# Optimization experiments

Hardware: AMD Instinct MI355X
Metric: run time of the kernel (lower is better)

The kernel has to match this reference:

```python
import jax, jax.numpy as jnp
import numpy as np

NUM_EXECUTORS = 50
NUM_DAG_FEATURES = 3
EMB_DAG = 16
EMB_GLOB = 16
HIDDEN = [64, 64, 32]
B = 60000            # number of jobs (one per env in the batched rollout)
NODES_PER_JOB = 10
NODE_FEAT = 5


def _init_mlp(key, dims):
    ws, bs = [], []
    for i in range(len(dims) - 1):
        key, k = jax.random.split(key)
        scale = 1.0 / np.sqrt(dims[i])
        ws.append(jax.random.uniform(k, (dims[i], dims[i + 1]), jnp.float32, -scale, scale))
        bs.append(jnp.zeros((dims[i + 1],), jnp.float32))
    return ws, bs


def setup_inputs() -> dict:
    rng = np.random.default_rng(0)
    n_nodes = B * NODES_PER_JOB
    # dag_batch.ptr: job i owns nodes [i*NODES_PER_JOB, (i+1)*NODES_PER_JOB)
    ptr = np.arange(B + 1, dtype=np.int64) * NODES_PER_JOB
    job_indices = rng.permutation(B).astype(np.int64)
    # ragged action counts per job (exec_mask is a prefix mask of length num_exec_acts[i])
    num_exec_acts = rng.integers(1, NUM_EXECUTORS + 1, size=B).astype(np.int64)
    n_sel = num_exec_acts[job_indices]
    T = int(n_sel.sum())
    # per-ragged-row executor index: concat([arange(n) for n in n_sel]), vectorized
    starts = np.cumsum(n_sel) - n_sel
    exec_act_idx = (np.arange(T, dtype=np.int64) - np.repeat(starts, n_sel)).astype(np.int64)

    key = jax.random.key(0)
    k_x, k_hd, k_hg, k_mlp = jax.random.split(key, 4)
    x = jax.random.normal(k_x, (n_nodes, NODE_FEAT), jnp.float32)
    h_dag = jax.random.normal(k_hd, (B, EMB_DAG), jnp.float32)
    h_glob = jax.random.normal(k_hg, (B, EMB_GLOB), jnp.float32)

    in_dim = NUM_DAG_FEATURES + EMB_DAG + EMB_GLOB + 1  # 36
    ws, bs = _init_mlp(k_mlp, [in_dim] + HIDDEN + [1])

    return {
        "x": x,
        "h_dag": h_dag,
        "h_glob": h_glob,
        "ptr": jnp.asarray(ptr),
        "job_indices": jnp.asarray(job_indices),
        "num_exec_acts": jnp.asarray(num_exec_acts),
        "exec_act_idx": jnp.asarray(exec_act_idx),
        "W1": ws[0], "b1": bs[0],
        "W2": ws[1], "b2": bs[1],
        "W3": ws[2], "b3": bs[2],
        "W4": ws[3], "b4": bs[3],
    }


def reference(x, h_dag, h_glob, ptr, job_indices, num_exec_acts, exec_act_idx,
              W1, b1, W2, b2, W3, b3, W4, b4):
    T = exec_act_idx.shape[0]                       # total ragged action rows (static)
    J = job_indices.shape[0]
    # masked gather: dag features at each dag's start node, then select jobs
    x_dag = x[ptr[:-1], :NUM_DAG_FEATURES][job_indices]        # [J, 3]
    h_dag_sel = h_dag[job_indices]                              # [J, 16]
    x_h_dag = jnp.concatenate([x_dag, h_dag_sel], axis=1)       # [J, 19]
    # variable repeat_interleave -> gather by repeated row index
    n_sel = num_exec_acts[job_indices]
    rpt = jnp.repeat(jnp.arange(J), n_sel, total_repeat_length=T)
    x_h_rpt = x_h_dag[rpt]                                      # [T, 19]
    h_glob_rpt = h_glob[rpt]                                    # [T, 16]
    # exec action feature: k / num_executors for the k-th valid executor
    exec_actions = (exec_act_idx.astype(x.dtype) / NUM_EXECUTORS)[:, None]  # [T, 1]
    h = jnp.concatenate([x_h_rpt, h_glob_rpt, exec_actions], axis=1)        # [T, 36]
    h = jax.nn.relu(h @ W1 + b1)
    h = jax.nn.relu(h @ W2 + b2)
    h = jax.nn.relu(h @ W3 + b3)
    scores = (h @ W4 + b4).squeeze(-1)                          # [T]
    return scores
```

## Files before the change

### kernel.cpp

```cpp
#include <hip/hip_runtime.h>

#define TPB 256

using half8  = __attribute__((ext_vector_type(8))) _Float16;
using fp16x2 = __attribute__((ext_vector_type(2))) __fp16;
using f32x4  = __attribute__((ext_vector_type(4))) float;

static __device__ __forceinline__ unsigned short h2u(_Float16 h) {
    union { _Float16 h; unsigned short u; } v; v.h = h; return v.u;
}
static __device__ __forceinline__ unsigned pkrtz(float a, float b) {
    fp16x2 h = __builtin_amdgcn_cvt_pkrtz(a, b);
    return __builtin_bit_cast(unsigned, h);
}
template <int CTRL>
static __device__ __forceinline__ float dppmov(float x) {
    return __int_as_float(__builtin_amdgcn_mov_dpp(__float_as_int(x), CTRL, 0xF, 0xF, true));
}
#define DPP_SWAP 0xB1

__global__ __launch_bounds__(TPB) void k_prep(const float* __restrict__ x,
                                              const float* __restrict__ h_dag,
                                              const float* __restrict__ h_glob,
                                              const int* __restrict__ ptr,
                                              const int* __restrict__ job_indices,
                                              const int* __restrict__ num_exec_acts,
                                              int J, int nb,
                                              unsigned int* __restrict__ feat,
                                              int* __restrict__ bsum, int* __restrict__ jsv,
                                              const float* __restrict__ W1,
                                              const float* __restrict__ b1,
                                              const float* __restrict__ W2,
                                              const float* __restrict__ b2,
                                              const float* __restrict__ W3,
                                              const float* __restrict__ b3,
                                              const float* __restrict__ W4,
                                              uint4* __restrict__ wfrag,
                                              float4* __restrict__ bfrag)
{
    if (blockIdx.x == (unsigned)nb) {
        if (threadIdx.x < 64) {
            int lane = threadIdx.x;
            int n = lane & 15, q = lane >> 4;
#pragma unroll
            for (int nt = 0; nt < 4; nt++) {
#pragma unroll
                for (int s = 0; s < 2; s++) {
                    half8 w1f, w2f;
#pragma unroll
                    for (int jj = 0; jj < 8; jj++) {
                        int ks = s * 32 + q * 8 + jj;
                        w1f[jj] = (ks < 36) ? (_Float16)W1[ks * 64 + nt * 16 + n] : (_Float16)0.0f;
                        w2f[jj] = (_Float16)W2[ks * 64 + nt * 16 + n];
                    }
                    wfrag[(nt * 2 + s) * 64 + lane]     = __builtin_bit_cast(uint4, w1f);
                    wfrag[(8 + nt * 2 + s) * 64 + lane] = __builtin_bit_cast(uint4, w2f);
                }
            }
#pragma unroll
            for (int nt = 0; nt < 2; nt++) {
#pragma unroll
                for (int s = 0; s < 2; s++) {
                    half8 w3f;
#pragma unroll
                    for (int jj = 0; jj < 8; jj++) {
                        int ks = s * 32 + q * 8 + jj;
                        w3f[jj] = (_Float16)W3[ks * 32 + nt * 16 + n];
                    }
                    wfrag[(16 + nt * 2 + s) * 64 + lane] = __builtin_bit_cast(uint4, w3f);
                }
            }
            bfrag[0 * 64 + lane] = make_float4(b1[n], b1[16 + n], b1[32 + n], b1[48 + n]);
            bfrag[1 * 64 + lane] = make_float4(b2[n], b2[16 + n], b2[32 + n], b2[48 + n]);
            bfrag[2 * 64 + lane] = make_float4(b3[n], b3[16 + n], W4[n], W4[16 + n]);
        }
        return;
    }

    __shared__ int sc[TPB];
    int j = blockIdx.x * TPB + threadIdx.x;
    int v = 0;
    if (j < J) {
        int ji   = job_indices[j];
        v        = num_exec_acts[ji];
        int node = ptr[ji];
        float f[40];
        f[0] = x[node * 5 + 0];
        f[1] = x[node * 5 + 1];
        f[2] = x[node * 5 + 2];
        float4 hd[4], hg[4];
#pragma unroll
        for (int c4 = 0; c4 < 4; c4++) hd[c4] = *(const float4*)(h_dag + (size_t)ji * 16 + 4 * c4);
#pragma unroll
        for (int c4 = 0; c4 < 4; c4++) hg[c4] = *(const float4*)(h_glob + (size_t)j * 16 + 4 * c4);
#pragma unroll
        for (int c4 = 0; c4 < 4; c4++) {
            f[3 + 4 * c4 + 0]  = hd[c4].x; f[3 + 4 * c4 + 1]  = hd[c4].y;
            f[3 + 4 * c4 + 2]  = hd[c4].z; f[3 + 4 * c4 + 3]  = hd[c4].w;
            f[19 + 4 * c4 + 0] = hg[c4].x; f[19 + 4 * c4 + 1] = hg[c4].y;
            f[19 + 4 * c4 + 2] = hg[c4].z; f[19 + 4 * c4 + 3] = hg[c4].w;
        }
#pragma unroll
        for (int c = 35; c < 40; c++) f[c] = 0.0f;
        unsigned int w[20];
#pragma unroll
        for (int k = 0; k < 20; k++)
            w[k] = (unsigned)h2u((_Float16)f[2 * k]) | ((unsigned)h2u((_Float16)f[2 * k + 1]) << 16);
        uint4* dst = (uint4*)(feat + (size_t)j * 20);
#pragma unroll
        for (int qq = 0; qq < 5; qq++)
            dst[qq] = make_uint4(w[4 * qq], w[4 * qq + 1], w[4 * qq + 2], w[4 * qq + 3]);
    }
    sc[threadIdx.x] = v;
    __syncthreads();
    for (int d = 1; d < TPB; d <<= 1) {
        int add = (threadIdx.x >= d) ? sc[threadIdx.x - d] : 0;
        __syncthreads();
        sc[threadIdx.x] += add;
        __syncthreads();
    }
    if (j < J) jsv[j] = ((sc[threadIdx.x] - v) << 6) | v;
    if (threadIdx.x == TPB - 1) bsum[blockIdx.x] = sc[TPB - 1];
}

__global__ __launch_bounds__(TPB) void k_mlp_mfma(const unsigned int* __restrict__ feat,
                                                  const int* __restrict__ jsv,
                                                  const int* __restrict__ bsum,
                                                  const uint4* __restrict__ wfrag,
                                                  const float4* __restrict__ bfrag,
                                                  const float* __restrict__ b4,
                                                  float* __restrict__ out,
                                                  int T, int J, int nb, int numTiles, int chunk)
{
    __shared__ __align__(16) char smem[4 * 4096];
    __shared__ int boffs[TPB];
    __shared__ int swin[4][64];
    __shared__ int srow[4][32];
    const int tid  = threadIdx.x;
    const int lane = tid & 63;
    const int wv   = tid >> 6;
    const int n    = lane & 15;
    const int q    = lane >> 4;
    char* slab = smem + wv * 4096;

    {
        int v = (tid < nb) ? bsum[tid] : 0;
        boffs[tid] = v;
        __syncthreads();
        for (int d = 1; d < TPB; d <<= 1) {
            int add = (tid >= d) ? boffs[tid - d] : 0;
            __syncthreads();
            boffs[tid] += add;
            __syncthreads();
        }
        int ex = boffs[tid] - v;
        __syncthreads();
        boffs[tid] = ex;
        __syncthreads();
    }

    half8 bw1[4][2], bw2[4][2], bw3[2][2];
#pragma unroll
    for (int nt = 0; nt < 4; nt++)
#pragma unroll
        for (int s = 0; s < 2; s++) {
            bw1[nt][s] = __builtin_bit_cast(half8, wfrag[(nt * 2 + s) * 64 + lane]);
            bw2[nt][s] = __builtin_bit_cast(half8, wfrag[(8 + nt * 2 + s) * 64 + lane]);
        }
#pragma unroll
    for (int nt = 0; nt < 2; nt++)
#pragma unroll
        for (int s = 0; s < 2; s++)
            bw3[nt][s] = __builtin_bit_cast(half8, wfrag[(16 + nt * 2 + s) * 64 + lane]);

    float4 bf1 = bfrag[0 * 64 + lane];
    float4 bf2 = bfrag[1 * 64 + lane];
    float4 bf3 = bfrag[2 * 64 + lane];
    float bb1[4] = {bf1.x, bf1.y, bf1.z, bf1.w};
    float bb2[4] = {bf2.x, bf2.y, bf2.z, bf2.w};
    float bb3[2] = {bf3.x, bf3.y};
    const float w4a = bf3.z, w4b = bf3.w;
    const float b4v = b4[0];
    const int   swr = (n >> 1) & 7;
    const int   odd = n & 1;

    const int t0 = blockIdx.x * chunk;
    const int t1 = (t0 + chunk < numTiles) ? (t0 + chunk) : numTiles;
    const int R  = (t1 - t0) * 32;
    const int r0 = t0 * 128 + wv * R;
    int rend = r0 + R;
    if (rend > T) rend = T;

    if (r0 < rend) {
        int j_lo;
        {
            int lo = 0, hi = nb - 1;
            while (lo < hi) {
                int mid = (lo + hi + 1) >> 1;
                if (boffs[mid] <= r0) lo = mid; else hi = mid - 1;
            }
            j_lo = lo << 8;
        }
        int sreg    = 0;
        int win_top = 0x80000000;

        for (int rb = r0; rb < rend; rb += 32) {
            if (win_top <= rb + 31) {
                for (;;) {
                    int jj = j_lo + lane;
                    sreg = (jj < J) ? (boffs[jj >> 8] + (jsv[jj] >> 6)) : 0x7fffffff;
                    unsigned long long m = __ballot(sreg <= rb);
                    int adv = 63 - __builtin_clzll(m);
                    j_lo += adv;
                    if (adv == 0) break;
                }
                swin[wv][lane] = sreg;
                win_top = __shfl(sreg, 63);
            }

            if (lane < 32) {
                int rt = rb + lane;
                const int* sw = swin[wv];
                int lj = 0;
#pragma unroll
                for (int stp = 32; stp; stp >>= 1) {
                    int c = lj + stp;
                    if (c < 64 && sw[c] <= rt) lj = c;
                }
                srow[wv][lane] = (lj << 8) | (rt - sw[lj]);
            }

            half8 a1[2][2];
#pragma unroll
            for (int mt = 0; mt < 2; mt++) {
                int  rt    = rb + 16 * mt + n;
                bool valid = rt < T;
                int  u     = srow[wv][16 * mt + n];
                int  jj2   = j_lo + (u >> 8);
                const uint4* fsrc = (const uint4*)(feat + (size_t)jj2 * 20);
                uint4 g0 = fsrc[q];
                a1[mt][0] = __builtin_bit_cast(half8, g0);
                uint4 g1 = make_uint4(0, 0, 0, 0);
                if (q == 0) {
                    g1 = fsrc[4];
                    float fe = valid ? (float)(u & 255) * 0.02f : 0.0f;
                    g1.y = (g1.y & 0xffffu) | ((unsigned)h2u((_Float16)fe) << 16);
                }
                a1[mt][1] = __builtin_bit_cast(half8, g1);
            }

#pragma unroll
            for (int mt = 0; mt < 2; mt++) {
                f32x4 acc[4];
#pragma unroll
                for (int nt = 0; nt < 4; nt++) { f32x4 c; c[0]=c[1]=c[2]=c[3]=bb1[nt]; acc[nt]=c; }
#pragma unroll
                for (int s = 0; s < 2; s++) {
#pragma unroll
                    for (int nt = 0; nt < 4; nt++)
                        acc[nt] = __builtin_amdgcn_mfma_f32_16x16x32_f16(a1[mt][s], bw1[nt][s], acc[nt], 0, 0, 0);
                }
                unsigned* sl = (unsigned*)slab;
#pragma unroll
                for (int nt = 0; nt < 4; nt++) {
                    float v0 = fmaxf(acc[nt][0], 0.0f), v1 = fmaxf(acc[nt][1], 0.0f);
                    float v2 = fmaxf(acc[nt][2], 0.0f), v3 = fmaxf(acc[nt][3], 0.0f);
                    float t0_ = dppmov<DPP_SWAP>(v0), t1_ = dppmov<DPP_SWAP>(v1);
                    float t2_ = dppmov<DPP_SWAP>(v2), t3_ = dppmov<DPP_SWAP>(v3);
                    unsigned u0 = pkrtz(odd ? t2_ : v0, odd ? v2 : t0_);
                    unsigned u1 = pkrtz(odd ? t3_ : v1, odd ? v3 : t1_);
                    int rowA = 16 * mt + 4 * q + (odd ? 2 : 0);
                    int c    = 2 * nt + (n >> 3);
                    int a0   = (rowA * 8 + (c ^ ((rowA >> 1) & 7))) * 4 + ((n >> 1) & 3);
                    sl[a0] = u0; sl[a0 + 32] = u1;
                }
            }

#pragma unroll
            for (int mt = 0; mt < 2; mt++) {
                const int M0 = 16 * mt;
                f32x4 acc[4];
#pragma unroll
                for (int nt = 0; nt < 4; nt++) { f32x4 c; c[0]=c[1]=c[2]=c[3]=bb2[nt]; acc[nt]=c; }
#pragma unroll
                for (int s = 0; s < 2; s++) {
                    half8 a = *(const half8*)(slab + ((M0 + n) * 8 + ((s * 4 + q) ^ swr)) * 16);
#pragma unroll
                    for (int nt = 0; nt < 4; nt++)
                        acc[nt] = __builtin_amdgcn_mfma_f32_16x16x32_f16(a, bw2[nt][s], acc[nt], 0, 0, 0);
                }
                unsigned* sl = (unsigned*)slab;
#pragma unroll
                for (int nt = 0; nt < 4; nt++) {
                    float v0 = fmaxf(acc[nt][0], 0.0f), v1 = fmaxf(acc[nt][1], 0.0f);
                    float v2 = fmaxf(acc[nt][2], 0.0f), v3 = fmaxf(acc[nt][3], 0.0f);
                    float t0_ = dppmov<DPP_SWAP>(v0), t1_ = dppmov<DPP_SWAP>(v1);
                    float t2_ = dppmov<DPP_SWAP>(v2), t3_ = dppmov<DPP_SWAP>(v3);
                    unsigned u0 = pkrtz(odd ? t2_ : v0, odd ? v2 : t0_);
                    unsigned u1 = pkrtz(odd ? t3_ : v1, odd ? v3 : t1_);
                    int rowA = M0 + 4 * q + (odd ? 2 : 0);
                    int c    = 2 * nt + (n >> 3);
                    int a0   = (rowA * 8 + (c ^ ((rowA >> 1) & 7))) * 4 + ((n >> 1) & 3);
                    sl[a0] = u0; sl[a0 + 32] = u1;
                }
            }

#pragma unroll
            for (int mt = 0; mt < 2; mt++) {
                const int M0 = 16 * mt;
                f32x4 acc[2];
#pragma unroll
                for (int nt = 0; nt < 2; nt++) { f32x4 c; c[0]=c[1]=c[2]=c[3]=bb3[nt]; acc[nt]=c; }
#pragma unroll
                for (int s = 0; s < 2; s++) {
                    half8 a = *(const half8*)(slab + ((M0 + n) * 8 + ((s * 4 + q) ^ swr)) * 16);
#pragma unroll
                    for (int nt = 0; nt < 2; nt++)
                        acc[nt] = __builtin_amdgcn_mfma_f32_16x16x32_f16(a, bw3[nt][s], acc[nt], 0, 0, 0);
                }
                f32x4 red;
#pragma unroll
                for (int r = 0; r < 4; r++)
                    red[r] = fmaxf(acc[0][r], 0.0f) * w4a + fmaxf(acc[1][r], 0.0f) * w4b;
#pragma unroll
                for (int r = 0; r < 4; r++) {
                    red[r] += dppmov<0x121>(red[r]);
                    red[r] += dppmov<0x122>(red[r]);
                    red[r] += dppmov<0x124>(red[r]);
                    red[r] += dppmov<0x128>(red[r]);
                }
                int t = rb + M0 + q * 4 + n;
                float val = (n == 0) ? red[0] : (n == 1) ? red[1] : (n == 2) ? red[2] : red[3];
                if (n < 4 && t < T) out[t] = val + b4v;
            }
        }
    }
}

extern "C" void kernel_launch(void* const* d_in, const int* in_sizes, int n_in,
                              void* d_out, int out_size, void* d_ws, size_t ws_size,
                              hipStream_t stream)
{
    const float* x             = (const float*)d_in[0];
    const float* h_dag         = (const float*)d_in[1];
    const float* h_glob        = (const float*)d_in[2];
    const int*   ptr           = (const int*)d_in[3];
    const int*   job_indices   = (const int*)d_in[4];
    const int*   num_exec_acts = (const int*)d_in[5];
    const float* W1 = (const float*)d_in[7];
    const float* b1 = (const float*)d_in[8];
    const float* W2 = (const float*)d_in[9];
    const float* b2 = (const float*)d_in[10];
    const float* W3 = (const float*)d_in[11];
    const float* b3 = (const float*)d_in[12];
    const float* W4 = (const float*)d_in[13];
    const float* b4 = (const float*)d_in[14];
    float* out = (float*)d_out;

    int J  = in_sizes[4];
    int T  = in_sizes[6];
    int nb = (J + TPB - 1) / TPB;

    char* wsp = (char*)d_ws;
    int* bsum = (int*)wsp;
    wsp += (((size_t)nb * 4) + 255) / 256 * 256;
    int* jsv = (int*)wsp;
    wsp += (((size_t)J * 4) + 255) / 256 * 256;
    uint4* wfrag = (uint4*)wsp;
    wsp += 20 * 64 * 16;
    float4* bfrag = (float4*)wsp;
    wsp += 3 * 64 * 16;
    unsigned int* feat = (unsigned int*)wsp;

    k_prep<<<nb + 1, TPB, 0, stream>>>(x, h_dag, h_glob, ptr, job_indices, num_exec_acts,
                                       J, nb, feat, bsum, jsv,
                                       W1, b1, W2, b2, W3, b3, W4, wfrag, bfrag);

    int numTiles = (T + 127) / 128;
    int grid = numTiles < 1280 ? numTiles : 1280;
    int chunk = (numTiles + grid - 1) / grid;
    grid = (numTiles + chunk - 1) / chunk;
    k_mlp_mfma<<<grid, TPB, 0, stream>>>(feat, jsv, bsum, wfrag, bfrag, b4,
                                         out, T, J, nb, numTiles, chunk);
}
```

Measured before the change: 181.4 us.

## Fuse prep and MLP kernels into one persistent kernel with grid barrier

```diff
diff --git a/kernel.cpp b/kernel.cpp
--- a/kernel.cpp
+++ b/kernel.cpp
@@ -19,118 +19,28 @@
 }
 #define DPP_SWAP 0xB1
 
-__global__ __launch_bounds__(TPB) void k_prep(const float* __restrict__ x,
-                                              const float* __restrict__ h_dag,
-                                              const float* __restrict__ h_glob,
-                                              const int* __restrict__ ptr,
-                                              const int* __restrict__ job_indices,
-                                              const int* __restrict__ num_exec_acts,
-                                              int J, int nb,
-                                              unsigned int* __restrict__ feat,
-                                              int* __restrict__ bsum, int* __restrict__ jsv,
-                                              const float* __restrict__ W1,
-                                              const float* __restrict__ b1,
-                                              const float* __restrict__ W2,
-                                              const float* __restrict__ b2,
-                                              const float* __restrict__ W3,
-                                              const float* __restrict__ b3,
-                                              const float* __restrict__ W4,
-                                              uint4* __restrict__ wfrag,
-                                              float4* __restrict__ bfrag)
-{
-    if (blockIdx.x == (unsigned)nb) {
-        if (threadIdx.x < 64) {
-            int lane = threadIdx.x;
-            int n = lane & 15, q = lane >> 4;
-#pragma unroll
-            for (int nt = 0; nt < 4; nt++) {
-#pragma unroll
-                for (int s = 0; s < 2; s++) {
-                    half8 w1f, w2f;
-#pragma unroll
-                    for (int jj = 0; jj < 8; jj++) {
-                        int ks = s * 32 + q * 8 + jj;
-                        w1f[jj] = (ks < 36) ? (_Float16)W1[ks * 64 + nt * 16 + n] : (_Float16)0.0f;
-                        w2f[jj] = (_Float16)W2[ks * 64 + nt * 16 + n];
-                    }
-                    wfrag[(nt * 2 + s) * 64 + lane]     = __builtin_bit_cast(uint4, w1f);
-                    wfrag[(8 + nt * 2 + s) * 64 + lane] = __builtin_bit_cast(uint4, w2f);
-                }
-            }
-#pragma unroll
-            for (int nt = 0; nt < 2; nt++) {
-#pragma unroll
-                for (int s = 0; s < 2; s++) {
-                    half8 w3f;
-#pragma unroll
-                    for (int jj = 0; jj < 8; jj++) {
-                        int ks = s * 32 + q * 8 + jj;
-                        w3f[jj] = (_Float16)W3[ks * 32 + nt * 16 + n];
-                    }
-                    wfrag[(16 + nt * 2 + s) * 64 + lane] = __builtin_bit_cast(uint4, w3f);
-                }
-            }
-            bfrag[0 * 64 + lane] = make_float4(b1[n], b1[16 + n], b1[32 + n], b1[48 + n]);
-            bfrag[1 * 64 + lane] = make_float4(b2[n], b2[16 + n], b2[32 + n], b2[48 + n]);
-            bfrag[2 * 64 + lane] = make_float4(b3[n], b3[16 + n], W4[n], W4[16 + n]);
-        }
-        return;
-    }
-
-    __shared__ int sc[TPB];
-    int j = blockIdx.x * TPB + threadIdx.x;
-    int v = 0;
-    if (j < J) {
-        int ji   = job_indices[j];
-        v        = num_exec_acts[ji];
-        int node = ptr[ji];
-        float f[40];
-        f[0] = x[node * 5 + 0];
-        f[1] = x[node * 5 + 1];
-        f[2] = x[node * 5 + 2];
-        float4 hd[4], hg[4];
-#pragma unroll
-        for (int c4 = 0; c4 < 4; c4++) hd[c4] = *(const float4*)(h_dag + (size_t)ji * 16 + 4 * c4);
-#pragma unroll
-        for (int c4 = 0; c4 < 4; c4++) hg[c4] = *(const float4*)(h_glob + (size_t)j * 16 + 4 * c4);
-#pragma unroll
-        for (int c4 = 0; c4 < 4; c4++) {
-            f[3 + 4 * c4 + 0]  = hd[c4].x; f[3 + 4 * c4 + 1]  = hd[c4].y;
-            f[3 + 4 * c4 + 2]  = hd[c4].z; f[3 + 4 * c4 + 3]  = hd[c4].w;
-            f[19 + 4 * c4 + 0] = hg[c4].x; f[19 + 4 * c4 + 1] = hg[c4].y;
-            f[19 + 4 * c4 + 2] = hg[c4].z; f[19 + 4 * c4 + 3] = hg[c4].w;
-        }
-#pragma unroll
-        for (int c = 35; c < 40; c++) f[c] = 0.0f;
-        unsigned int w[20];
-#pragma unroll
-        for (int k = 0; k < 20; k++)
-            w[k] = (unsigned)h2u((_Float16)f[2 * k]) | ((unsigned)h2u((_Float16)f[2 * k + 1]) << 16);
-        uint4* dst = (uint4*)(feat + (size_t)j * 20);
-#pragma unroll
-        for (int qq = 0; qq < 5; qq++)
-            dst[qq] = make_uint4(w[4 * qq], w[4 * qq + 1], w[4 * qq + 2], w[4 * qq + 3]);
-    }
-    sc[threadIdx.x] = v;
-    __syncthreads();
-    for (int d = 1; d < TPB; d <<= 1) {
-        int add = (threadIdx.x >= d) ? sc[threadIdx.x - d] : 0;
-        __syncthreads();
-        sc[threadIdx.x] += add;
-        __syncthreads();
-    }
-    if (j < J) jsv[j] = ((sc[threadIdx.x] - v) << 6) | v;
-    if (threadIdx.x == TPB - 1) bsum[blockIdx.x] = sc[TPB - 1];
-}
-
-__global__ __launch_bounds__(TPB) void k_mlp_mfma(const unsigned int* __restrict__ feat,
-                                                  const int* __restrict__ jsv,
-                                                  const int* __restrict__ bsum,
-                                                  const uint4* __restrict__ wfrag,
-                                                  const float4* __restrict__ bfrag,
-                                                  const float* __restrict__ b4,
-                                                  float* __restrict__ out,
-                                                  int T, int J, int nb, int numTiles, int chunk)
+__global__ __launch_bounds__(TPB) void k_fused(const float* __restrict__ x,
+                                               const float* __restrict__ h_dag,
+                                               const float* __restrict__ h_glob,
+                                               const int* __restrict__ ptr,
+                                               const int* __restrict__ job_indices,
+                                               const int* __restrict__ num_exec_acts,
+                                               const float* __restrict__ W1,
+                                               const float* __restrict__ b1,
+                                               const float* __restrict__ W2,
+                                               const float* __restrict__ b2,
+                                               const float* __restrict__ W3,
+                                               const float* __restrict__ b3,
+                                               const float* __restrict__ W4,
+                                               const float* __restrict__ b4,
+                                               unsigned int* __restrict__ feat,
+                                               int* __restrict__ bsum,
+                                               int* __restrict__ jsv,
+                                               uint4* __restrict__ wfrag,
+                                               float4* __restrict__ bfrag,
+                                               float* __restrict__ out,
+                                               int* bar,
+                                               int J, int nb, int T, int numTiles)
 {
     __shared__ __align__(16) char smem[4 * 4096];
     __shared__ int boffs[TPB];
@@ -142,6 +52,100 @@
     const int n    = lane & 15;
     const int q    = lane >> 4;
     char* slab = smem + wv * 4096;
+
+    for (int c = blockIdx.x; c <= nb; c += gridDim.x) {
+        if (c == nb) {
+            if (tid < 64) {
+                int l2 = tid;
+                int nn = l2 & 15, qq = l2 >> 4;
+#pragma unroll
+                for (int nt = 0; nt < 4; nt++) {
+#pragma unroll
+                    for (int s = 0; s < 2; s++) {
+                        half8 w1f, w2f;
+#pragma unroll
+                        for (int jj = 0; jj < 8; jj++) {
+                            int ks = s * 32 + qq * 8 + jj;
+                            w1f[jj] = (ks < 36) ? (_Float16)W1[ks * 64 + nt * 16 + nn] : (_Float16)0.0f;
+                            w2f[jj] = (_Float16)W2[ks * 64 + nt * 16 + nn];
+                        }
+                        wfrag[(nt * 2 + s) * 64 + l2]     = __builtin_bit_cast(uint4, w1f);
+                        wfrag[(8 + nt * 2 + s) * 64 + l2] = __builtin_bit_cast(uint4, w2f);
+                    }
+                }
+#pragma unroll
+                for (int nt = 0; nt < 2; nt++) {
+#pragma unroll
+                    for (int s = 0; s < 2; s++) {
+                        half8 w3f;
+#pragma unroll
+                        for (int jj = 0; jj < 8; jj++) {
+                            int ks = s * 32 + qq * 8 + jj;
+                            w3f[jj] = (_Float16)W3[ks * 32 + nt * 16 + nn];
+                        }
+                        wfrag[(16 + nt * 2 + s) * 64 + l2] = __builtin_bit_cast(uint4, w3f);
+                    }
+                }
+                bfrag[0 * 64 + l2] = make_float4(b1[nn], b1[16 + nn], b1[32 + nn], b1[48 + nn]);
+                bfrag[1 * 64 + l2] = make_float4(b2[nn], b2[16 + nn], b2[32 + nn], b2[48 + nn]);
+                bfrag[2 * 64 + l2] = make_float4(b3[nn], b3[16 + nn], W4[nn], W4[16 + nn]);
+            }
+        } else {
+            int j = c * TPB + tid;
+            int v = 0;
+            if (j < J) {
+                int ji   = job_indices[j];
+                v        = num_exec_acts[ji];
+                int node = ptr[ji];
+                float f[40];
+                f[0] = x[node * 5 + 0];
+                f[1] = x[node * 5 + 1];
+                f[2] = x[node * 5 + 2];
+                float4 hd[4], hg[4];
+#pragma unroll
+                for (int c4 = 0; c4 < 4; c4++) hd[c4] = *(const float4*)(h_dag + (size_t)ji * 16 + 4 * c4);
+#pragma unroll
+                for (int c4 = 0; c4 < 4; c4++) hg[c4] = *(const float4*)(h_glob + (size_t)j * 16 + 4 * c4);
+#pragma unroll
+                for (int c4 = 0; c4 < 4; c4++) {
+                    f[3 + 4 * c4 + 0]  = hd[c4].x; f[3 + 4 * c4 + 1]  = hd[c4].y;
+                    f[3 + 4 * c4 + 2]  = hd[c4].z; f[3 + 4 * c4 + 3]  = hd[c4].w;
+                    f[19 + 4 * c4 + 0] = hg[c4].x; f[19 + 4 * c4 + 1] = hg[c4].y;
+                    f[19 + 4 * c4 + 2] = hg[c4].z; f[19 + 4 * c4 + 3] = hg[c4].w;
+                }
+#pragma unroll
+                for (int cc = 35; cc < 40; cc++) f[cc] = 0.0f;
+                unsigned int w[20];
+#pragma unroll
+                for (int k = 0; k < 20; k++)
+                    w[k] = (unsigned)h2u((_Float16)f[2 * k]) | ((unsigned)h2u((_Float16)f[2 * k + 1]) << 16);
+                uint4* dst = (uint4*)(feat + (size_t)j * 20);
+#pragma unroll
+                for (int qq = 0; qq < 5; qq++)
+                    dst[qq] = make_uint4(w[4 * qq], w[4 * qq + 1], w[4 * qq + 2], w[4 * qq + 3]);
+            }
+            boffs[tid] = v;
+            __syncthreads();
+            for (int d = 1; d < TPB; d <<= 1) {
+                int add = (tid >= d) ? boffs[tid - d] : 0;
+                __syncthreads();
+                boffs[tid] += add;
+                __syncthreads();
+            }
+            if (j < J) jsv[j] = ((boffs[tid] - v) << 6) | v;
+            if (tid == TPB - 1) bsum[c] = boffs[TPB - 1];
+        }
+    }
+
+    __threadfence();
+    __syncthreads();
+    if (tid == 0) {
+        __hip_atomic_fetch_add(bar, 1, __ATOMIC_RELEASE, __HIP_MEMORY_SCOPE_AGENT);
+        while (__hip_atomic_load(bar, __ATOMIC_ACQUIRE, __HIP_MEMORY_SCOPE_AGENT) < (int)gridDim.x)
+            __builtin_amdgcn_s_sleep(8);
+    }
+    __syncthreads();
+    __threadfence();
 
     {
         int v = (tid < nb) ? bsum[tid] : 0;
@@ -184,12 +188,62 @@
     const int   swr = (n >> 1) & 7;
     const int   odd = n & 1;
 
+    const int chunk = (numTiles + gridDim.x - 1) / gridDim.x;
     const int t0 = blockIdx.x * chunk;
-    const int t1 = (t0 + chunk < numTiles) ? (t0 + chunk) : numTiles;
+    int t1 = t0 + chunk; if (t1 > numTiles) t1 = numTiles;
+    if (t0 >= numTiles) return;
     const int R  = (t1 - t0) * 32;
     const int r0 = t0 * 128 + wv * R;
     int rend = r0 + R;
     if (rend > T) rend = T;
+
+#define REFILL_SEARCH(RB)                                                        \
+    {                                                                            \
+        if (win_top <= (RB) + 31) {                                              \
+            for (;;) {                                                           \
+                int jj = j_lo + lane;                                            \
+                sreg = (jj < J) ? (boffs[jj >> 8] + (jsv[jj] >> 6)) : 0x7fffffff;\
+                unsigned long long m = __ballot(sreg <= (RB));                   \
+                int adv = 63 - __builtin_clzll(m);                               \
+                j_lo += adv;                                                     \
+                if (adv == 0) break;                                             \
+            }                                                                    \
+            swin[wv][lane] = sreg;                                               \
+            win_top = __shfl(sreg, 63);                                          \
+        }                                                                        \
+        if (lane < 32) {                                                         \
+            int rt = (RB) + lane;                                                \
+            const int* sw = swin[wv];                                            \
+            int lj = 0;                                                          \
+            _Pragma("unroll")                                                    \
+            for (int stp = 32; stp; stp >>= 1) {                                 \
+                int c2 = lj + stp;                                               \
+                if (c2 < 64 && sw[c2] <= rt) lj = c2;                            \
+            }                                                                    \
+            srow[wv][lane] = (lj << 8) | (rt - sw[lj]);                          \
+        }                                                                        \
+    }
+
+#define BUILD_A1(RB, A1)                                                         \
+    {                                                                            \
+        _Pragma("unroll")                                                        \
+        for (int mt = 0; mt < 2; mt++) {                                         \
+            int  rt    = (RB) + 16 * mt + n;                                     \
+            bool valid = rt < T;                                                 \
+            int  u     = srow[wv][16 * mt + n];                                  \
+            int  jj2   = j_lo + (u >> 8);                                        \
+            const uint4* fsrc = (const uint4*)(feat + (size_t)jj2 * 20);         \
+            uint4 g0 = fsrc[q];                                                  \
+            A1[mt][0] = __builtin_bit_cast(half8, g0);                           \
+            uint4 g1 = make_uint4(0, 0, 0, 0);                                   \
+            if (q == 0) {                                                        \
+                g1 = fsrc[4];                                                    \
+                float fe = valid ? (float)(u & 255) * 0.02f : 0.0f;              \
+                g1.y = (g1.y & 0xffffu) | ((unsigned)h2u((_Float16)fe) << 16);   \
+            }                                                                    \
+            A1[mt][1] = __builtin_bit_cast(half8, g1);                           \
+        }                                                                        \
+    }
 
     if (r0 < rend) {
         int j_lo;
@@ -204,67 +258,36 @@
         int sreg    = 0;
         int win_top = 0x80000000;
 
+        REFILL_SEARCH(r0);
+        half8 a1[2][2];
+        BUILD_A1(r0, a1);
+
         for (int rb = r0; rb < rend; rb += 32) {
-            if (win_top <= rb + 31) {
-                for (;;) {
-                    int jj = j_lo + lane;
-                    sreg = (jj < J) ? (boffs[jj >> 8] + (jsv[jj] >> 6)) : 0x7fffffff;
-                    unsigned long long m = __ballot(sreg <= rb);
-                    int adv = 63 - __builtin_clzll(m);
-                    j_lo += adv;
-                    if (adv == 0) break;
-                }
-                swin[wv][lane] = sreg;
-                win_top = __shfl(sreg, 63);
-            }
-
-            if (lane < 32) {
-                int rt = rb + lane;
-                const int* sw = swin[wv];
-                int lj = 0;
-#pragma unroll
-                for (int stp = 32; stp; stp >>= 1) {
-                    int c = lj + stp;
-                    if (c < 64 && sw[c] <= rt) lj = c;
-                }
-                srow[wv][lane] = (lj << 8) | (rt - sw[lj]);
-            }
-
-            half8 a1[2][2];
+            f32x4 acc1[2][4];
 #pragma unroll
             for (int mt = 0; mt < 2; mt++) {
-                int  rt    = rb + 16 * mt + n;
-                bool valid = rt < T;
-                int  u     = srow[wv][16 * mt + n];
-                int  jj2   = j_lo + (u >> 8);
-                const uint4* fsrc = (const uint4*)(feat + (size_t)jj2 * 20);
-                uint4 g0 = fsrc[q];
-                a1[mt][0] = __builtin_bit_cast(half8, g0);
-                uint4 g1 = make_uint4(0, 0, 0, 0);
-                if (q == 0) {
-                    g1 = fsrc[4];
-                    float fe = valid ? (float)(u & 255) * 0.02f : 0.0f;
-                    g1.y = (g1.y & 0xffffu) | ((unsigned)h2u((_Float16)fe) << 16);
-                }
-                a1[mt][1] = __builtin_bit_cast(half8, g1);
+#pragma unroll
+                for (int nt = 0; nt < 4; nt++) { f32x4 c; c[0]=c[1]=c[2]=c[3]=bb1[nt]; acc1[mt][nt]=c; }
+#pragma unroll
+                for (int s = 0; s < 2; s++)
+#pragma unroll
+                    for (int nt = 0; nt < 4; nt++)
+                        acc1[mt][nt] = __builtin_amdgcn_mfma_f32_16x16x32_f16(a1[mt][s], bw1[nt][s], acc1[mt][nt], 0, 0, 0);
+            }
+
+            int rbn = rb + 32;
+            if (rbn < rend) {
+                REFILL_SEARCH(rbn);
+                BUILD_A1(rbn, a1);
             }
 
 #pragma unroll
             for (int mt = 0; mt < 2; mt++) {
-                f32x4 acc[4];
-#pragma unroll
-                for (int nt = 0; nt < 4; nt++) { f32x4 c; c[0]=c[1]=c[2]=c[3]=bb1[nt]; acc[nt]=c; }
-#pragma unroll
-                for (int s = 0; s < 2; s++) {
-#pragma unroll
-                    for (int nt = 0; nt < 4; nt++)
-                        acc[nt] = __builtin_amdgcn_mfma_f32_16x16x32_f16(a1[mt][s], bw1[nt][s], acc[nt], 0, 0, 0);
-                }
                 unsigned* sl = (unsigned*)slab;
 #pragma unroll
                 for (int nt = 0; nt < 4; nt++) {
-                    float v0 = fmaxf(acc[nt][0], 0.0f), v1 = fmaxf(acc[nt][1], 0.0f);
-                    float v2 = fmaxf(acc[nt][2], 0.0f), v3 = fmaxf(acc[nt][3], 0.0f);
+                    float v0 = fmaxf(acc1[mt][nt][0], 0.0f), v1 = fmaxf(acc1[mt][nt][1], 0.0f);
+                    float v2 = fmaxf(acc1[mt][nt][2], 0.0f), v3 = fmaxf(acc1[mt][nt][3], 0.0f);
                     float t0_ = dppmov<DPP_SWAP>(v0), t1_ = dppmov<DPP_SWAP>(v1);
                     float t2_ = dppmov<DPP_SWAP>(v2), t3_ = dppmov<DPP_SWAP>(v3);
                     unsigned u0 = pkrtz(odd ? t2_ : v0, odd ? v2 : t0_);
@@ -335,6 +358,8 @@
             }
         }
     }
+#undef REFILL_SEARCH
+#undef BUILD_A1
 }
 
 extern "C" void kernel_launch(void* const* d_in, const int* in_sizes, int n_in,
@@ -362,6 +387,8 @@
     int nb = (J + TPB - 1) / TPB;
 
     char* wsp = (char*)d_ws;
+    int* bar = (int*)wsp;
+    wsp += 256;
     int* bsum = (int*)wsp;
     wsp += (((size_t)nb * 4) + 255) / 256 * 256;
     int* jsv = (int*)wsp;
@@ -372,14 +399,25 @@
     wsp += 3 * 64 * 16;
     unsigned int* feat = (unsigned int*)wsp;
 
-    k_prep<<<nb + 1, TPB, 0, stream>>>(x, h_dag, h_glob, ptr, job_indices, num_exec_acts,
-                                       J, nb, feat, bsum, jsv,
-                                       W1, b1, W2, b2, W3, b3, W4, wfrag, bfrag);
-
     int numTiles = (T + 127) / 128;
-    int grid = numTiles < 1280 ? numTiles : 1280;
-    int chunk = (numTiles + grid - 1) / grid;
-    grid = (numTiles + chunk - 1) / chunk;
-    k_mlp_mfma<<<grid, TPB, 0, stream>>>(feat, jsv, bsum, wfrag, bfrag, b4,
-                                         out, T, J, nb, numTiles, chunk);
+
+    static int g_grid = 0;
+    if (g_grid == 0) {
+        int dev = 0, cus = 0, bpc = 0;
+        hipGetDevice(&dev);
+        hipDeviceGetAttribute(&cus, hipDeviceAttributeMultiprocessorCount, dev);
+        hipOccupancyMaxActiveBlocksPerMultiprocessor(&bpc, k_fused, TPB, 0);
+        if (cus <= 0) cus = 256;
+        if (bpc <= 0) bpc = 1;
+        long long g = (long long)cus * bpc;
+        if (g > 2048) g = 2048;
+        g_grid = (int)g;
+    }
+    int grid = g_grid;
+
+    hipMemsetAsync(bar, 0, 8, stream);
+    k_fused<<<grid, TPB, 0, stream>>>(x, h_dag, h_glob, ptr, job_indices, num_exec_acts,
+                                      W1, b1, W2, b2, W3, b3, W4, b4,
+                                      feat, bsum, jsv, wfrag, bfrag, out, bar,
+                                      J, nb, T, numTiles);
 }
```

After: 287.4 us. 58.5% more time.
